# Optimization experiments

Hardware: AMD Instinct MI355X
Metric: run time of the kernel (lower is better)

The kernel has to match this reference:

```python
import jax, jax.numpy as jnp
import numpy as np

NA = 3            # anchors per scale
NC = 80           # num classes
THRESH = 0.6      # wh-IoU anchor-match threshold
EPS = 1e-7

ANCHORS_PX = np.array([[12,16],[19,36],[40,28],[36,75],[76,55],[72,146],
                       [142,110],[192,243],[459,401]], dtype=np.float32).reshape(3, 3, 2)


def setup_inputs() -> dict:
    key = jax.random.key(0)
    k1, k2, k3, k4, k5, k6 = jax.random.split(key, 6)
    B, M = 16, 32
    p0 = jax.random.normal(k1, (B, NA * (5 + NC), 80, 80), jnp.float32)
    p1 = jax.random.normal(k2, (B, NA * (5 + NC), 40, 40), jnp.float32)
    p2 = jax.random.normal(k3, (B, NA * (5 + NC), 20, 20), jnp.float32)
    # targets: [B, M, 6] = (img_idx, class in [1,NC], cx, cy, w, h) normalized to [0,1]
    bidx = jnp.broadcast_to(jnp.arange(B, dtype=jnp.float32)[:, None], (B, M))
    cls = jax.random.randint(k4, (B, M), 1, NC + 1).astype(jnp.float32)
    xy = jax.random.uniform(k5, (B, M, 2), minval=0.05, maxval=0.95)
    ka, kj = jax.random.split(k6)
    aidx = jax.random.randint(ka, (B, M), 0, 9)
    base_wh = jnp.asarray(ANCHORS_PX.reshape(9, 2))[aidx] / 640.0
    jitter = jnp.exp(jax.random.uniform(kj, (B, M, 2), minval=-0.15, maxval=0.15))
    wh = base_wh * jitter
    targets = jnp.concatenate([bidx[..., None], cls[..., None], xy, wh], axis=-1)
    return {"p0": p0, "p1": p1, "p2": p2,
            "targets": targets,
            "anchors": jnp.asarray(ANCHORS_PX),
            "image_size": jnp.array([640.0, 640.0], jnp.float32)}


def _bce_logits(x, t):
    # BCEWithLogits, pos_weight=1, elementwise
    return jnp.maximum(x, 0.0) - x * t + jnp.log1p(jnp.exp(-jnp.abs(x)))


def _giou(pbox, tbox):
    # boxes [N,4] in cxcywh
    px1 = pbox[:, 0] - pbox[:, 2] * 0.5
    py1 = pbox[:, 1] - pbox[:, 3] * 0.5
    px2 = pbox[:, 0] + pbox[:, 2] * 0.5
    py2 = pbox[:, 1] + pbox[:, 3] * 0.5
    tx1 = tbox[:, 0] - tbox[:, 2] * 0.5
    ty1 = tbox[:, 1] - tbox[:, 3] * 0.5
    tx2 = tbox[:, 0] + tbox[:, 2] * 0.5
    ty2 = tbox[:, 1] + tbox[:, 3] * 0.5
    iw = jnp.clip(jnp.minimum(px2, tx2) - jnp.maximum(px1, tx1), 0.0)
    ih = jnp.clip(jnp.minimum(py2, ty2) - jnp.maximum(py1, ty1), 0.0)
    inter = iw * ih
    union = pbox[:, 2] * pbox[:, 3] + tbox[:, 2] * tbox[:, 3] - inter + EPS
    iou = inter / union
    cw = jnp.maximum(px2, tx2) - jnp.minimum(px1, tx1)
    ch = jnp.maximum(py2, ty2) - jnp.minimum(py1, ty1)
    c_area = cw * ch + EPS
    return iou - (c_area - union) / c_area


def _scale_losses(pi, tflat, anchors_i, image_size):
    # pi: [B, NA*(5+NC), H, W]; tflat: [N,6]; anchors_i: [NA,2] in pixels
    B = pi.shape[0]
    H, W = pi.shape[-2:]
    stride = image_size / jnp.array([H, W], jnp.float32)          # (sH, sW)
    anchor = anchors_i / stride[::-1][None, :]                    # anchors in grid units (w,h)
    gain = jnp.concatenate([jnp.ones((2,), jnp.float32),
                            (1.0 / stride)[jnp.array([1, 0, 1, 0])]])
    t = tflat * gain                                              # [N,6]
    gwh = t[:, 4:6]
    # wh-IoU matrix [NA, N] -> best anchor per target
    inter = (jnp.minimum(anchor[:, None, 0], gwh[None, :, 0])
             * jnp.minimum(anchor[:, None, 1], gwh[None, :, 1]))
    union = anchor[:, None, 0] * anchor[:, None, 1] + gwh[None, :, 0] * gwh[None, :, 1] - inter
    iou = inter / union
    best = iou.max(0)
    a = iou.argmax(0)
    mask = best > THRESH                                          # fixed-shape mask replaces torch boolean compaction
    maskf = mask.astype(jnp.float32)

    b = jnp.where(mask, t[:, 0].astype(jnp.int32), 0)
    c = t[:, 1].astype(jnp.int32)
    gxy = t[:, 2:4]
    gi = jnp.where(mask, gxy[:, 0].astype(jnp.int32), 0)
    gj = jnp.where(mask, gxy[:, 1].astype(jnp.int32), 0)
    a_s = jnp.where(mask, a, 0)

    pir = pi.reshape(B, NA, 5 + NC, H, W).transpose(0, 1, 3, 4, 2)  # [B,NA,H,W,5+NC]
    ps = pir[b, a_s, gj, gi]                                        # [N,5+NC]
    tobj = jnp.zeros((B, NA, H, W), jnp.float32)
    tobj = tobj.at[b, a_s, gj, gi].max(jax.lax.stop_gradient(maskf))

    pxy = jax.nn.sigmoid(ps[:, 0:2])
    pwh = jnp.minimum(jnp.exp(ps[:, 2:4]), 1000.0) * anchor[a_s]
    pbox = jnp.concatenate([pxy, pwh], 1)
    tbox = jnp.concatenate([gxy % 1.0, t[:, 4:6]], 1)
    giou = _giou(pbox, tbox)
    nb = jnp.maximum(maskf.sum(), 1.0)
    lbox = (maskf * (1.0 - giou)).sum() / nb
    tcls = jax.nn.one_hot(c - 1, NC, dtype=jnp.float32)             # cp=1, cn=0 (eps=0)
    lcls = (maskf[:, None] * _bce_logits(ps[:, 5:], tcls)).sum() / (nb * NC)
    lobj = _bce_logits(pir[..., 4], tobj).mean()
    return lbox, lobj, lcls


def _total_loss(p0, p1, p2, targets, anchors, image_size):
    tflat = targets.reshape(-1, 6)
    lbox = lobj = lcls = jnp.float32(0.0)
    for i, pi in enumerate([p0, p1, p2]):
        lb, lo, lc = _scale_losses(pi, tflat, anchors[i], image_size)
        lbox = lbox + lb
        lobj = lobj + lo
        lcls = lcls + lc
    lbox = lbox * 3.54
    lobj = lobj * 64.3
    lcls = lcls * 37.4
    return lbox + lobj + lcls, lbox, lobj, lcls


def reference(p0, p1, p2, targets, anchors, image_size):
    return _total_loss(p0, p1, p2, targets, anchors, image_size)
```

## Files before the change

### kernel.cpp

```cpp
#include <hip/hip_runtime.h>
#include <math.h>

#define NAANCH 3
#define NCLS 80
#define BATCH 16
#define MTGT 32
#define NTGT (BATCH * MTGT)
#define CH (5 + NCLS)

__device__ __forceinline__ float bce0(float x) {
    return fmaxf(x, 0.0f) + log1pf(expf(-fabsf(x)));
}
__device__ __forceinline__ float bce(float x, float t) {
    return fmaxf(x, 0.0f) - x * t + log1pf(expf(-fabsf(x)));
}

__global__ void assign_kernel(const float* __restrict__ p0,
                              const float* __restrict__ p1,
                              const float* __restrict__ p2,
                              const float* __restrict__ targets,
                              const float* __restrict__ anchors,
                              const float* __restrict__ image_size,
                              float* __restrict__ ws) {
    const int s = blockIdx.x;
    const int j = threadIdx.x;
    const int H = (s == 0) ? 80 : ((s == 1) ? 40 : 20);
    const int W = H;
    const float* pi = (s == 0) ? p0 : ((s == 1) ? p1 : p2);

    const float img0 = image_size[0], img1 = image_size[1];
    const float stride0 = img0 / (float)H;
    const float stride1 = img1 / (float)W;
    const float gx = 1.0f / stride1;
    const float gy = 1.0f / stride0;

    __shared__ int   keys[NTGT];
    __shared__ unsigned char mk[NTGT];
    __shared__ float wpart[4][8];

    const float t0 = targets[j * 6 + 0];
    const float t1 = targets[j * 6 + 1];
    const float tx = targets[j * 6 + 2] * gx;
    const float ty = targets[j * 6 + 3] * gy;
    const float gw = targets[j * 6 + 4] * gx;
    const float gh = targets[j * 6 + 5] * gy;

    float best = -1.0f; int abest = 0;
    for (int k = 0; k < NAANCH; ++k) {
        float aw = anchors[(s * NAANCH + k) * 2 + 0] / stride1;
        float ah = anchors[(s * NAANCH + k) * 2 + 1] / stride0;
        float inter = fminf(aw, gw) * fminf(ah, gh);
        float uni = aw * ah + gw * gh - inter;
        float iou = inter / uni;
        if (iou > best) { best = iou; abest = k; }
    }
    const bool  mask  = best > 0.6f;
    const float maskf = mask ? 1.0f : 0.0f;

    int b  = mask ? (int)t0 : 0;
    const int c = (int)t1;
    int gi = mask ? (int)tx : 0;
    int gj = mask ? (int)ty : 0;
    const int a_s = mask ? abest : 0;
    gi = min(max(gi, 0), W - 1);
    gj = min(max(gj, 0), H - 1);
    b  = min(max(b, 0), BATCH - 1);

    float lbox_t = 0.0f, lcls_t = 0.0f, ps4 = 0.0f;
    const int key = ((b * NAANCH + a_s) * H + gj) * W + gi;

    if (mask) {
        const int HW = H * W;
        const float* base = pi + (size_t)(b * (NAANCH * CH) + a_s * CH) * HW + gj * W + gi;
        const float ps0 = base[0 * HW];
        const float ps1 = base[1 * HW];
        const float ps2 = base[2 * HW];
        const float ps3 = base[3 * HW];
        ps4 = base[4 * HW];

        const float aw = anchors[(s * NAANCH + a_s) * 2 + 0] / stride1;
        const float ah = anchors[(s * NAANCH + a_s) * 2 + 1] / stride0;

        const float pxc = 1.0f / (1.0f + expf(-ps0));
        const float pyc = 1.0f / (1.0f + expf(-ps1));
        const float pw  = fminf(expf(ps2), 1000.0f) * aw;
        const float ph  = fminf(expf(ps3), 1000.0f) * ah;
        const float txc = tx - floorf(tx);
        const float tyc = ty - floorf(ty);

        const float px1 = pxc - pw * 0.5f, py1 = pyc - ph * 0.5f;
        const float px2 = pxc + pw * 0.5f, py2 = pyc + ph * 0.5f;
        const float qx1 = txc - gw * 0.5f, qy1 = tyc - gh * 0.5f;
        const float qx2 = txc + gw * 0.5f, qy2 = tyc + gh * 0.5f;
        const float iw = fmaxf(fminf(px2, qx2) - fmaxf(px1, qx1), 0.0f);
        const float ih = fmaxf(fminf(py2, qy2) - fmaxf(py1, qy1), 0.0f);
        const float inter = iw * ih;
        const float uni = pw * ph + gw * gh - inter + 1e-7f;
        const float iou = inter / uni;
        const float cw = fmaxf(px2, qx2) - fminf(px1, qx1);
        const float chh = fmaxf(py2, qy2) - fminf(py1, qy1);
        const float carea = cw * chh + 1e-7f;
        const float giou = iou - (carea - uni) / carea;
        lbox_t = 1.0f - giou;

        const int ci = c - 1;
        float sum = 0.0f;
        for (int k = 0; k < NCLS; ++k) {
            float x = base[(5 + k) * HW];
            sum += bce(x, (k == ci) ? 1.0f : 0.0f);
        }
        lcls_t = sum;
    }

    keys[j] = key; mk[j] = mask ? 1 : 0;
    __syncthreads();

    float corr = 0.0f;
    if (mask) {
        bool dup = false;
        for (int j2 = 0; j2 < j; ++j2)
            if (mk[j2] && keys[j2] == key) { dup = true; break; }
        if (!dup) corr = -ps4;
    }

    float vals[4] = { lbox_t, maskf, lcls_t, corr };
    const int lane = j & 63, wid = j >> 6;
    for (int q = 0; q < 4; ++q) {
        float v = vals[q];
        for (int off = 32; off > 0; off >>= 1) v += __shfl_down(v, off, 64);
        if (lane == 0) wpart[q][wid] = v;
    }
    __syncthreads();
    if (j == 0) {
        float acc[4];
        for (int q = 0; q < 4; ++q) {
            float v = 0.0f;
            for (int w2 = 0; w2 < 8; ++w2) v += wpart[q][w2];
            acc[q] = v;
        }
        ws[0 + s]  = 0.0f;
        ws[3 + s]  = acc[0];
        ws[6 + s]  = acc[1];
        ws[9 + s]  = acc[2];
        ws[12 + s] = acc[3];
    }
}

template <int HW>
__device__ __forceinline__ float obj_elem(const float* __restrict__ pi, int e) {
    int ba = e / HW;
    int hw = e - ba * HW;
    int b  = ba / NAANCH;
    int a  = ba - b * NAANCH;
    float x = pi[(size_t)(b * (NAANCH * CH) + a * CH + 4) * HW + hw];
    return bce0(x);
}

__global__ void obj_kernel(const float* __restrict__ p0,
                           const float* __restrict__ p1,
                           const float* __restrict__ p2,
                           float* __restrict__ ws) {
    const int blk = blockIdx.x;
    const int tid = threadIdx.x;
    float v; int s;
    if (blk < 1200)      { s = 0; v = obj_elem<6400>(p0, blk * 256 + tid); }
    else if (blk < 1500) { s = 1; v = obj_elem<1600>(p1, (blk - 1200) * 256 + tid); }
    else                 { s = 2; v = obj_elem<400 >(p2, (blk - 1500) * 256 + tid); }

    for (int off = 32; off > 0; off >>= 1) v += __shfl_down(v, off, 64);
    __shared__ float part[4];
    const int lane = tid & 63, wid = tid >> 6;
    if (lane == 0) part[wid] = v;
    __syncthreads();
    if (tid == 0) {
        atomicAdd(&ws[s], part[0] + part[1] + part[2] + part[3]);
    }
}

__global__ void finalize_kernel(const float* __restrict__ ws, float* __restrict__ out) {
    if (threadIdx.x == 0 && blockIdx.x == 0) {
        const float Ns[3] = { 307200.0f, 76800.0f, 19200.0f };
        float lbox = 0.0f, lobj = 0.0f, lcls = 0.0f;
        for (int s = 0; s < 3; ++s) {
            float nb = fmaxf(ws[6 + s], 1.0f);
            lbox += ws[3 + s] / nb;
            lobj += (ws[0 + s] + ws[12 + s]) / Ns[s];
            lcls += ws[9 + s] / (nb * (float)NCLS);
        }
        lbox *= 3.54f; lobj *= 64.3f; lcls *= 37.4f;
        out[0] = lbox + lobj + lcls;
        out[1] = lbox;
        out[2] = lobj;
        out[3] = lcls;
    }
}

extern "C" void kernel_launch(void* const* d_in, const int* in_sizes, int n_in,
                              void* d_out, int out_size, void* d_ws, size_t ws_size,
                              hipStream_t stream) {
    const float* p0       = (const float*)d_in[0];
    const float* p1       = (const float*)d_in[1];
    const float* p2       = (const float*)d_in[2];
    const float* targets  = (const float*)d_in[3];
    const float* anchors  = (const float*)d_in[4];
    const float* img_size = (const float*)d_in[5];
    float* out = (float*)d_out;
    float* ws  = (float*)d_ws;

    assign_kernel<<<3, NTGT, 0, stream>>>(p0, p1, p2, targets, anchors, img_size, ws);
    obj_kernel<<<1575, 256, 0, stream>>>(p0, p1, p2, ws);
    finalize_kernel<<<1, 64, 0, stream>>>(ws, out);
}
```

Measured before the change: 173.4 us.

## Fuse assign and objectness kernels, parallelize class BCE per wave, vectorize obj loads

Merges the target-assignment and objectness kernels into one launch. Three blocks handle assignment, and the remaining blocks read the objectness channel with float4 loads. The 80-class BCE per matched target is now spread across the lanes of a wave with coalesced-per-wave reads, instead of a serial 80-iteration loop per thread. Objectness partial sums are written per block and reduced in finalize, removing the atomics and the ws[0..2] zeroing dependency. The cost is fewer, heavier blocks: only 197 objectness blocks, which may underfill the GPU's compute units.

```diff
diff --git a/kernel.cpp b/kernel.cpp
--- a/kernel.cpp
+++ b/kernel.cpp
@@ -4,187 +4,234 @@
 #define NAANCH 3
 #define NCLS 80
 #define BATCH 16
-#define MTGT 32
-#define NTGT (BATCH * MTGT)
-#define CH (5 + NCLS)
+#define NTGT 512
+#define CH 85
+
+#define V4_S0 76800
+#define V4_S1 19200
+#define V4_S2 4800
+#define V4_TOT (V4_S0 + V4_S1 + V4_S2)
+#define OBJ_BLOCKS 197
 
 __device__ __forceinline__ float bce0(float x) {
     return fmaxf(x, 0.0f) + log1pf(expf(-fabsf(x)));
 }
-__device__ __forceinline__ float bce(float x, float t) {
-    return fmaxf(x, 0.0f) - x * t + log1pf(expf(-fabsf(x)));
-}
-
-__global__ void assign_kernel(const float* __restrict__ p0,
-                              const float* __restrict__ p1,
-                              const float* __restrict__ p2,
-                              const float* __restrict__ targets,
-                              const float* __restrict__ anchors,
-                              const float* __restrict__ image_size,
-                              float* __restrict__ ws) {
-    const int s = blockIdx.x;
-    const int j = threadIdx.x;
-    const int H = (s == 0) ? 80 : ((s == 1) ? 40 : 20);
-    const int W = H;
-    const float* pi = (s == 0) ? p0 : ((s == 1) ? p1 : p2);
-
-    const float img0 = image_size[0], img1 = image_size[1];
-    const float stride0 = img0 / (float)H;
-    const float stride1 = img1 / (float)W;
-    const float gx = 1.0f / stride1;
-    const float gy = 1.0f / stride0;
-
-    __shared__ int   keys[NTGT];
-    __shared__ unsigned char mk[NTGT];
-    __shared__ float wpart[4][8];
-
-    const float t0 = targets[j * 6 + 0];
-    const float t1 = targets[j * 6 + 1];
-    const float tx = targets[j * 6 + 2] * gx;
-    const float ty = targets[j * 6 + 3] * gy;
-    const float gw = targets[j * 6 + 4] * gx;
-    const float gh = targets[j * 6 + 5] * gy;
-
-    float best = -1.0f; int abest = 0;
-    for (int k = 0; k < NAANCH; ++k) {
-        float aw = anchors[(s * NAANCH + k) * 2 + 0] / stride1;
-        float ah = anchors[(s * NAANCH + k) * 2 + 1] / stride0;
-        float inter = fminf(aw, gw) * fminf(ah, gh);
-        float uni = aw * ah + gw * gh - inter;
-        float iou = inter / uni;
-        if (iou > best) { best = iou; abest = k; }
+
+__device__ __forceinline__ float wave_sum(float v) {
+    for (int off = 32; off > 0; off >>= 1) v += __shfl_down(v, off, 64);
+    return v;
+}
+
+__global__ void fused_kernel(const float* __restrict__ p0,
+                             const float* __restrict__ p1,
+                             const float* __restrict__ p2,
+                             const float* __restrict__ targets,
+                             const float* __restrict__ anchors,
+                             const float* __restrict__ image_size,
+                             float* __restrict__ ws) {
+    const int tid  = threadIdx.x;
+    const int lane = tid & 63;
+    const int wid  = tid >> 6;
+
+    __shared__ int   sh_key[NTGT];
+    __shared__ int   sh_off[NTGT];
+    __shared__ int   sh_ci[NTGT];
+    __shared__ unsigned char sh_mk[NTGT];
+    __shared__ float red[4][8];
+
+    if (blockIdx.x < 3) {
+        const int s = blockIdx.x;
+        const int j = tid;
+        const int H = (s == 0) ? 80 : ((s == 1) ? 40 : 20);
+        const int W = H;
+        const int HW = H * W;
+        const float* pi = (s == 0) ? p0 : ((s == 1) ? p1 : p2);
+
+        const float stride0 = image_size[0] / (float)H;
+        const float stride1 = image_size[1] / (float)W;
+        const float gx = 1.0f / stride1;
+        const float gy = 1.0f / stride0;
+
+        const float t0 = targets[j * 6 + 0];
+        const float t1 = targets[j * 6 + 1];
+        const float tx = targets[j * 6 + 2] * gx;
+        const float ty = targets[j * 6 + 3] * gy;
+        const float gw = targets[j * 6 + 4] * gx;
+        const float gh = targets[j * 6 + 5] * gy;
+
+        float best = -1.0f; int abest = 0;
+        for (int k = 0; k < NAANCH; ++k) {
+            float aw = anchors[(s * NAANCH + k) * 2 + 0] / stride1;
+            float ah = anchors[(s * NAANCH + k) * 2 + 1] / stride0;
+            float inter = fminf(aw, gw) * fminf(ah, gh);
+            float uni = aw * ah + gw * gh - inter;
+            float iou = inter / uni;
+            if (iou > best) { best = iou; abest = k; }
+        }
+        const bool  mask  = best > 0.6f;
+        const float maskf = mask ? 1.0f : 0.0f;
+
+        int b  = mask ? (int)t0 : 0;
+        const int c = (int)t1;
+        int gi = mask ? (int)tx : 0;
+        int gj = mask ? (int)ty : 0;
+        const int a_s = mask ? abest : 0;
+        gi = min(max(gi, 0), W - 1);
+        gj = min(max(gj, 0), H - 1);
+        b  = min(max(b, 0), BATCH - 1);
+
+        const int key = ((b * NAANCH + a_s) * H + gj) * W + gi;
+        const int off = (b * (NAANCH * CH) + a_s * CH) * HW + gj * W + gi;
+
+        float lbox_t = 0.0f, ps4 = 0.0f;
+        if (mask) {
+            const float ps0 = pi[off + 0 * HW];
+            const float ps1 = pi[off + 1 * HW];
+            const float ps2 = pi[off + 2 * HW];
+            const float ps3 = pi[off + 3 * HW];
+            ps4 = pi[off + 4 * HW];
+
+            const float aw = anchors[(s * NAANCH + a_s) * 2 + 0] / stride1;
+            const float ah = anchors[(s * NAANCH + a_s) * 2 + 1] / stride0;
+
+            const float pxc = 1.0f / (1.0f + expf(-ps0));
+            const float pyc = 1.0f / (1.0f + expf(-ps1));
+            const float pw  = fminf(expf(ps2), 1000.0f) * aw;
+            const float ph  = fminf(expf(ps3), 1000.0f) * ah;
+            const float txc = tx - floorf(tx);
+            const float tyc = ty - floorf(ty);
+
+            const float px1 = pxc - pw * 0.5f, py1 = pyc - ph * 0.5f;
+            const float px2 = pxc + pw * 0.5f, py2 = pyc + ph * 0.5f;
+            const float qx1 = txc - gw * 0.5f, qy1 = tyc - gh * 0.5f;
+            const float qx2 = txc + gw * 0.5f, qy2 = tyc + gh * 0.5f;
+            const float iw = fmaxf(fminf(px2, qx2) - fmaxf(px1, qx1), 0.0f);
+            const float ih = fmaxf(fminf(py2, qy2) - fmaxf(py1, qy1), 0.0f);
+            const float inter = iw * ih;
+            const float uni = pw * ph + gw * gh - inter + 1e-7f;
+            const float iou = inter / uni;
+            const float cw  = fmaxf(px2, qx2) - fminf(px1, qx1);
+            const float chh = fmaxf(py2, qy2) - fminf(py1, qy1);
+            const float carea = cw * chh + 1e-7f;
+            lbox_t = 1.0f - (iou - (carea - uni) / carea);
+        }
+
+        sh_key[j] = key;
+        sh_off[j] = off;
+        sh_ci[j]  = c - 1;
+        sh_mk[j]  = mask ? 1 : 0;
+        __syncthreads();
+
+        float corr = 0.0f;
+        if (mask) {
+            bool dup = false;
+            for (int j2 = 0; j2 < j; ++j2)
+                if (sh_mk[j2] && sh_key[j2] == key) { dup = true; break; }
+            if (!dup) corr = -ps4;
+        }
+
+        float v0 = wave_sum(lbox_t);
+        float v1 = wave_sum(maskf);
+        float v2 = wave_sum(corr);
+        if (lane == 0) { red[0][wid] = v0; red[1][wid] = v1; red[2][wid] = v2; }
+        __syncthreads();
+
+        float lcls_w = 0.0f;
+        for (int j2 = wid; j2 < NTGT; j2 += 8) {
+            if (!sh_mk[j2]) continue;
+            const int toff = sh_off[j2];
+            const int ci   = sh_ci[j2];
+            const int k1 = lane;
+            float x1 = pi[toff + (5 + k1) * HW];
+            float c1 = bce0(x1) - ((k1 == ci) ? x1 : 0.0f);
+            float c2 = 0.0f;
+            if (lane < NCLS - 64) {
+                const int k2 = 64 + lane;
+                float x2 = pi[toff + (5 + k2) * HW];
+                c2 = bce0(x2) - ((k2 == ci) ? x2 : 0.0f);
+            }
+            float tsum = wave_sum(c1 + c2);
+            if (lane == 0) lcls_w += tsum;
+        }
+        if (lane == 0) red[3][wid] = lcls_w;
+        __syncthreads();
+
+        if (tid == 0) {
+            float acc[4] = {0.f, 0.f, 0.f, 0.f};
+            for (int w = 0; w < 8; ++w) {
+                acc[0] += red[0][w]; acc[1] += red[1][w];
+                acc[2] += red[2][w]; acc[3] += red[3][w];
+            }
+            ws[3 + s]  = acc[0];
+            ws[6 + s]  = acc[1];
+            ws[9 + s]  = acc[3];
+            ws[12 + s] = acc[2];
+        }
+    } else {
+        const int vb = (blockIdx.x - 3) * 512 + tid;
+        float a0 = 0.f, a1 = 0.f, a2 = 0.f;
+        if (vb < V4_TOT) {
+            const float4* addr; int hw4; int sflag;
+            if (vb < V4_S0) {
+                const int u = vb;
+                const int ba = u / 1600;  hw4 = u - ba * 1600;
+                const int b = ba / 3, a = ba - 3 * b;
+                addr = (const float4*)(p0 + (size_t)((b * NAANCH + a) * CH + 4) * 6400);
+                sflag = 0;
+            } else if (vb < V4_S0 + V4_S1) {
+                const int u = vb - V4_S0;
+                const int ba = u / 400;   hw4 = u - ba * 400;
+                const int b = ba / 3, a = ba - 3 * b;
+                addr = (const float4*)(p1 + (size_t)((b * NAANCH + a) * CH + 4) * 1600);
+                sflag = 1;
+            } else {
+                const int u = vb - V4_S0 - V4_S1;
+                const int ba = u / 100;   hw4 = u - ba * 100;
+                const int b = ba / 3, a = ba - 3 * b;
+                addr = (const float4*)(p2 + (size_t)((b * NAANCH + a) * CH + 4) * 400);
+                sflag = 2;
+            }
+            float4 x = addr[hw4];
+            float v = bce0(x.x) + bce0(x.y) + bce0(x.z) + bce0(x.w);
+            if (sflag == 0) a0 = v; else if (sflag == 1) a1 = v; else a2 = v;
+        }
+        a0 = wave_sum(a0); a1 = wave_sum(a1); a2 = wave_sum(a2);
+        if (lane == 0) { red[0][wid] = a0; red[1][wid] = a1; red[2][wid] = a2; }
+        __syncthreads();
+        if (tid == 0) {
+            float s0 = 0.f, s1 = 0.f, s2 = 0.f;
+            for (int w = 0; w < 8; ++w) { s0 += red[0][w]; s1 += red[1][w]; s2 += red[2][w]; }
+            const int blk = blockIdx.x - 3;
+            ws[16 + blk * 3 + 0] = s0;
+            ws[16 + blk * 3 + 1] = s1;
+            ws[16 + blk * 3 + 2] = s2;
+        }
     }
-    const bool  mask  = best > 0.6f;
-    const float maskf = mask ? 1.0f : 0.0f;
-
-    int b  = mask ? (int)t0 : 0;
-    const int c = (int)t1;
-    int gi = mask ? (int)tx : 0;
-    int gj = mask ? (int)ty : 0;
-    const int a_s = mask ? abest : 0;
-    gi = min(max(gi, 0), W - 1);
-    gj = min(max(gj, 0), H - 1);
-    b  = min(max(b, 0), BATCH - 1);
-
-    float lbox_t = 0.0f, lcls_t = 0.0f, ps4 = 0.0f;
-    const int key = ((b * NAANCH + a_s) * H + gj) * W + gi;
-
-    if (mask) {
-        const int HW = H * W;
-        const float* base = pi + (size_t)(b * (NAANCH * CH) + a_s * CH) * HW + gj * W + gi;
-        const float ps0 = base[0 * HW];
-        const float ps1 = base[1 * HW];
-        const float ps2 = base[2 * HW];
-        const float ps3 = base[3 * HW];
-        ps4 = base[4 * HW];
-
-        const float aw = anchors[(s * NAANCH + a_s) * 2 + 0] / stride1;
-        const float ah = anchors[(s * NAANCH + a_s) * 2 + 1] / stride0;
-
-        const float pxc = 1.0f / (1.0f + expf(-ps0));
-        const float pyc = 1.0f / (1.0f + expf(-ps1));
-        const float pw  = fminf(expf(ps2), 1000.0f) * aw;
-        const float ph  = fminf(expf(ps3), 1000.0f) * ah;
-        const float txc = tx - floorf(tx);
-        const float tyc = ty - floorf(ty);
-
-        const float px1 = pxc - pw * 0.5f, py1 = pyc - ph * 0.5f;
-        const float px2 = pxc + pw * 0.5f, py2 = pyc + ph * 0.5f;
-        const float qx1 = txc - gw * 0.5f, qy1 = tyc - gh * 0.5f;
-        const float qx2 = txc + gw * 0.5f, qy2 = tyc + gh * 0.5f;
-        const float iw = fmaxf(fminf(px2, qx2) - fmaxf(px1, qx1), 0.0f);
-        const float ih = fmaxf(fminf(py2, qy2) - fmaxf(py1, qy1), 0.0f);
-        const float inter = iw * ih;
-        const float uni = pw * ph + gw * gh - inter + 1e-7f;
-        const float iou = inter / uni;
-        const float cw = fmaxf(px2, qx2) - fminf(px1, qx1);
-        const float chh = fmaxf(py2, qy2) - fminf(py1, qy1);
-        const float carea = cw * chh + 1e-7f;
-        const float giou = iou - (carea - uni) / carea;
-        lbox_t = 1.0f - giou;
-
-        const int ci = c - 1;
-        float sum = 0.0f;
-        for (int k = 0; k < NCLS; ++k) {
-            float x = base[(5 + k) * HW];
-            sum += bce(x, (k == ci) ? 1.0f : 0.0f);
-        }
-        lcls_t = sum;
+}
+
+__global__ void finalize_kernel(const float* __restrict__ ws, float* __restrict__ out) {
+    const int t = threadIdx.x;
+    const int lane = t & 63, wid = t >> 6;
+    float o0 = 0.f, o1 = 0.f, o2 = 0.f;
+    if (t < OBJ_BLOCKS) {
+        o0 = ws[16 + t * 3 + 0];
+        o1 = ws[16 + t * 3 + 1];
+        o2 = ws[16 + t * 3 + 2];
     }
-
-    keys[j] = key; mk[j] = mask ? 1 : 0;
+    o0 = wave_sum(o0); o1 = wave_sum(o1); o2 = wave_sum(o2);
+    __shared__ float part[3][4];
+    if (lane == 0) { part[0][wid] = o0; part[1][wid] = o1; part[2][wid] = o2; }
     __syncthreads();
-
-    float corr = 0.0f;
-    if (mask) {
-        bool dup = false;
-        for (int j2 = 0; j2 < j; ++j2)
-            if (mk[j2] && keys[j2] == key) { dup = true; break; }
-        if (!dup) corr = -ps4;
-    }
-
-    float vals[4] = { lbox_t, maskf, lcls_t, corr };
-    const int lane = j & 63, wid = j >> 6;
-    for (int q = 0; q < 4; ++q) {
-        float v = vals[q];
-        for (int off = 32; off > 0; off >>= 1) v += __shfl_down(v, off, 64);
-        if (lane == 0) wpart[q][wid] = v;
-    }
-    __syncthreads();
-    if (j == 0) {
-        float acc[4];
-        for (int q = 0; q < 4; ++q) {
-            float v = 0.0f;
-            for (int w2 = 0; w2 < 8; ++w2) v += wpart[q][w2];
-            acc[q] = v;
-        }
-        ws[0 + s]  = 0.0f;
-        ws[3 + s]  = acc[0];
-        ws[6 + s]  = acc[1];
-        ws[9 + s]  = acc[2];
-        ws[12 + s] = acc[3];
-    }
-}
-
-template <int HW>
-__device__ __forceinline__ float obj_elem(const float* __restrict__ pi, int e) {
-    int ba = e / HW;
-    int hw = e - ba * HW;
-    int b  = ba / NAANCH;
-    int a  = ba - b * NAANCH;
-    float x = pi[(size_t)(b * (NAANCH * CH) + a * CH + 4) * HW + hw];
-    return bce0(x);
-}
-
-__global__ void obj_kernel(const float* __restrict__ p0,
-                           const float* __restrict__ p1,
-                           const float* __restrict__ p2,
-                           float* __restrict__ ws) {
-    const int blk = blockIdx.x;
-    const int tid = threadIdx.x;
-    float v; int s;
-    if (blk < 1200)      { s = 0; v = obj_elem<6400>(p0, blk * 256 + tid); }
-    else if (blk < 1500) { s = 1; v = obj_elem<1600>(p1, (blk - 1200) * 256 + tid); }
-    else                 { s = 2; v = obj_elem<400 >(p2, (blk - 1500) * 256 + tid); }
-
-    for (int off = 32; off > 0; off >>= 1) v += __shfl_down(v, off, 64);
-    __shared__ float part[4];
-    const int lane = tid & 63, wid = tid >> 6;
-    if (lane == 0) part[wid] = v;
-    __syncthreads();
-    if (tid == 0) {
-        atomicAdd(&ws[s], part[0] + part[1] + part[2] + part[3]);
-    }
-}
-
-__global__ void finalize_kernel(const float* __restrict__ ws, float* __restrict__ out) {
-    if (threadIdx.x == 0 && blockIdx.x == 0) {
+    if (t == 0) {
+        float obj[3];
+        for (int s = 0; s < 3; ++s)
+            obj[s] = part[s][0] + part[s][1] + part[s][2] + part[s][3];
         const float Ns[3] = { 307200.0f, 76800.0f, 19200.0f };
-        float lbox = 0.0f, lobj = 0.0f, lcls = 0.0f;
+        float lbox = 0.f, lobj = 0.f, lcls = 0.f;
         for (int s = 0; s < 3; ++s) {
             float nb = fmaxf(ws[6 + s], 1.0f);
             lbox += ws[3 + s] / nb;
-            lobj += (ws[0 + s] + ws[12 + s]) / Ns[s];
+            lobj += (obj[s] + ws[12 + s]) / Ns[s];
             lcls += ws[9 + s] / (nb * (float)NCLS);
         }
         lbox *= 3.54f; lobj *= 64.3f; lcls *= 37.4f;
@@ -207,7 +254,6 @@
     float* out = (float*)d_out;
     float* ws  = (float*)d_ws;
 
-    assign_kernel<<<3, NTGT, 0, stream>>>(p0, p1, p2, targets, anchors, img_size, ws);
-    obj_kernel<<<1575, 256, 0, stream>>>(p0, p1, p2, ws);
-    finalize_kernel<<<1, 64, 0, stream>>>(ws, out);
-}
+    fused_kernel<<<3 + OBJ_BLOCKS, 512, 0, stream>>>(p0, p1, p2, targets, anchors, img_size, ws);
+    finalize_kernel<<<1, 256, 0, stream>>>(ws, out);
+}
```

Result: faster. 155.0 us (-10.6%).
